# Kernel optimization log

Hardware: AMD Instinct MI355X
Metric: run time of the kernel (lower is better)

The kernel has to match this reference:

```python
import jax, jax.numpy as jnp
import numpy as np
from jax import lax

B, C, H, W_DIM, K = 8, 256, 128, 128, 64


def setup_inputs() -> dict:
    key = jax.random.key(0)
    k1, k2, k3, k4 = jax.random.split(key, 4)
    x = jax.random.normal(k1, (B, C, H, W_DIM), dtype=jnp.float32)
    index = jax.random.randint(k2, (B, H, W_DIM), 0, K)
    stdv = 1.0 / np.sqrt(C)
    W = jax.random.uniform(k3, (C, C), minval=-stdv, maxval=stdv, dtype=jnp.float32)
    conv_w = jax.random.normal(k4, (C, C, 1, 1), dtype=jnp.float32) * stdv
    return {"x": x, "index": index, "W": W, "conv_w": conv_w}


def reference(x, index, W, conv_w):
    # one-hot segment membership (B,H,W,K) -- replaces scatter_ + broadcast in torch
    onehot = jax.nn.one_hot(index, K, dtype=x.dtype)
    counts = jnp.sum(onehot, axis=(1, 2))                       # (B,K)
    sums = jnp.einsum('bhwk,bchw->bkc', onehot, x)              # segment sums
    denom = counts + (counts == 0).astype(x.dtype)              # avoid div by 0
    means = sums / denom[..., None]                             # (B,K,C)

    # Mahalanobis-style pairwise adjacency: adj[b,i,j] = exp(-d^T (W W^T) d)
    M = W @ W.T                                                 # (C,C)
    diff = means[:, None, :, :] - means[:, :, None, :]          # (B,K,K,C): means[b,j]-means[b,i]
    quad = jnp.einsum('bijc,cd,bijd->bij', diff, M, diff)
    adj = jnp.exp(-quad)
    adj = adj * (1.0 - jnp.eye(K, dtype=x.dtype))               # zero diagonal

    # adjacency-weighted message aggregation over segments
    agg = jnp.einsum('bij,bjc->bic', adj, means)                # (B,K,C)

    # scatter messages back to pixels by segment id (each pixel belongs to 1 segment)
    gathered = agg[jnp.arange(B)[:, None, None], index]         # (B,H,W,C)
    features = x + jnp.transpose(gathered, (0, 3, 1, 2))        # (B,C,H,W)

    # 1x1 conv, no bias
    out = lax.conv_general_dilated(features, conv_w, window_strides=(1, 1),
                                   padding='VALID',
                                   dimension_numbers=('NCHW', 'OIHW', 'NCHW'))
    return out
```

## Files before the change

### kernel.cpp

```cpp
#include <hip/hip_runtime.h>
#include <cstdint>
#include <cstddef>

#define B_  8
#define C_  256
#define HW_ 16384
#define K_  64

typedef __attribute__((ext_vector_type(8))) short bf16x8;
typedef __attribute__((ext_vector_type(4))) float f32x4;

__device__ __forceinline__ unsigned f2bf(float f) {
    unsigned u = __builtin_bit_cast(unsigned, f);
    return (u + 0x7FFFu + ((u >> 16) & 1u)) >> 16;
}
__device__ __forceinline__ float bf2f(unsigned h) {
    unsigned u = h << 16;
    return __builtin_bit_cast(float, u);
}

__global__ __launch_bounds__(256) void k_scatter(const float* __restrict__ x,
                                                 const int* __restrict__ idx,
                                                 float* __restrict__ part,
                                                 float* __restrict__ pcnt) {
    __shared__ float lsum[K_ * C_];
    __shared__ int   sidx[256];
    __shared__ float lcnt[K_];
    const int tid = threadIdx.x;
    const int b = blockIdx.y;
    const int pb = blockIdx.x;
    const int p0 = pb * 256;

    float4 z4 = make_float4(0.f, 0.f, 0.f, 0.f);
    for (int i = tid; i < K_ * C_ / 4; i += 256) ((float4*)lsum)[i] = z4;
    if (tid < K_) lcnt[tid] = 0.f;
    sidx[tid] = idx[b * HW_ + p0 + tid];
    __syncthreads();

    atomicAdd(&lcnt[sidx[tid]], 1.f);

    const int c = tid;
    const float4* xr = (const float4*)(x + ((size_t)b * C_ + c) * HW_ + p0);
    #pragma unroll 4
    for (int p4 = 0; p4 < 64; ++p4) {
        float4 v = xr[p4];
        int k0 = sidx[p4 * 4 + 0];
        int k1 = sidx[p4 * 4 + 1];
        int k2 = sidx[p4 * 4 + 2];
        int k3 = sidx[p4 * 4 + 3];
        atomicAdd(&lsum[k0 * C_ + c], v.x);
        atomicAdd(&lsum[k1 * C_ + c], v.y);
        atomicAdd(&lsum[k2 * C_ + c], v.z);
        atomicAdd(&lsum[k3 * C_ + c], v.w);
    }
    __syncthreads();

    const size_t pbg = (size_t)b * 64 + pb;
    float* dst = part + (pbg * K_) * C_;
    for (int k = 0; k < K_; ++k)
        dst[k * C_ + c] = lsum[k * C_ + c];
    if (tid < K_) pcnt[pbg * K_ + tid] = lcnt[tid];
}

__global__ __launch_bounds__(256) void k_reduce(const float* __restrict__ part,
                                                const float* __restrict__ pcnt,
                                                float* __restrict__ means) {
    const int bk = blockIdx.x;
    const int b = bk >> 6, k = bk & 63;
    const int c = threadIdx.x;
    __shared__ float cnt_s;

    if (c < 64) {
        float cl = pcnt[((size_t)b * 64 + c) * K_ + k];
        #pragma unroll
        for (int off = 32; off; off >>= 1) cl += __shfl_down(cl, off);
        if (c == 0) cnt_s = cl;
    }
    __syncthreads();
    const float cnt = cnt_s;
    const float denom = cnt + (cnt == 0.f ? 1.f : 0.f);

    float acc = 0.f;
    #pragma unroll 4
    for (int pb = 0; pb < 64; ++pb)
        acc += part[(((size_t)b * 64 + pb) * K_ + k) * C_ + c];
    means[(size_t)bk * C_ + c] = acc / denom;
}

__global__ __launch_bounds__(256) void k_prep(const float* __restrict__ Wm,
                                              const float* __restrict__ convw,
                                              float* __restrict__ Mm,
                                              float* __restrict__ cwT) {
    const int bx = blockIdx.x, t = threadIdx.x;
    __shared__ float wl[C_];
    if (bx < C_) {
        int cr = bx;
        wl[t] = Wm[cr * C_ + t];
        __syncthreads();
        float acc = 0.f;
        for (int e = 0; e < C_; ++e) acc += wl[e] * Wm[t * C_ + e];
        Mm[cr * C_ + t] = acc;
    } else {
        int cr = bx - C_;
        cwT[cr * C_ + t] = convw[t * C_ + cr];
    }
}

__global__ __launch_bounds__(256) void k_P(const float* __restrict__ means,
                                           const float* __restrict__ Mm,
                                           float* __restrict__ P) {
    const int bi = blockIdx.x;
    const int d = threadIdx.x;
    __shared__ float ml[C_];
    ml[d] = means[(size_t)bi * C_ + d];
    __syncthreads();
    float acc = 0.f;
    for (int cc = 0; cc < C_; ++cc) acc += ml[cc] * Mm[cc * C_ + d];
    P[(size_t)bi * C_ + d] = acc;
}

__global__ __launch_bounds__(256) void k_G(const float* __restrict__ P,
                                           const float* __restrict__ means,
                                           float* __restrict__ G) {
    const int bi = blockIdx.x;
    const int b = bi >> 6;
    const int t = threadIdx.x;
    __shared__ float pl[C_], ml[C_];
    pl[t] = P[(size_t)bi * C_ + t];
    ml[t] = means[(size_t)bi * C_ + t];
    __syncthreads();
    const int j = t >> 2, q = t & 3;
    const float* Pj = P + ((size_t)b * K_ + j) * C_ + q * 64;
    const float* mj = means + ((size_t)b * K_ + j) * C_ + q * 64;
    const float* pq = pl + q * 64;
    const float* mq = ml + q * 64;
    float acc = 0.f;
    for (int d0 = 0; d0 < 64; ++d0) {
        int d = (d0 + q * 16) & 63;
        acc += (pq[d] - Pj[d]) * (mq[d] - mj[d]);
    }
    acc += __shfl_xor(acc, 1);
    acc += __shfl_xor(acc, 2);
    if (q == 0) G[(size_t)bi * K_ + j] = acc;
}

__global__ __launch_bounds__(256) void k_agg(const float* __restrict__ G,
                                             const float* __restrict__ means,
                                             float* __restrict__ agg) {
    const int bi = blockIdx.x;
    const int b = bi >> 6, i = bi & 63;
    const int t = threadIdx.x;
    __shared__ float adjl[K_];
    if (t < K_) {
        int j = t;
        float quad = G[(size_t)bi * K_ + j];
        adjl[j] = (j == i) ? 0.f : expf(-quad);
    }
    __syncthreads();
    float acc = 0.f;
    for (int j = 0; j < K_; ++j)
        acc += adjl[j] * means[((size_t)b * K_ + j) * C_ + t];
    agg[(size_t)bi * C_ + t] = acc;
}

__global__ __launch_bounds__(256) void k_proj(const float* __restrict__ agg,
                                              const float* __restrict__ cwT,
                                              float* __restrict__ proj) {
    const int bk = blockIdx.x;
    const int o = threadIdx.x;
    __shared__ float al[C_];
    al[o] = agg[(size_t)bk * C_ + o];
    __syncthreads();
    float acc = 0.f;
    for (int cc = 0; cc < C_; ++cc) acc += al[cc] * cwT[cc * C_ + o];
    proj[(size_t)bk * C_ + o] = acc;
}

#define BM 128
#define BN 128
#define BKK 32
#define STRD 80

__global__ __launch_bounds__(256) void k_gemm(const float* __restrict__ x,
                                              const int* __restrict__ idx,
                                              const float* __restrict__ convw,
                                              const float* __restrict__ proj,
                                              float* __restrict__ out) {
    __shared__ float Xf[BKK][BN];
    __shared__ __align__(16) unsigned char AsH[BM * STRD];
    __shared__ __align__(16) unsigned char AsL[BM * STRD];
    __shared__ __align__(16) unsigned char BsH[BN * STRD];
    __shared__ __align__(16) unsigned char BsL[BN * STRD];

    const int tid = threadIdx.x;
    const int o0 = blockIdx.x * BM;
    const int p0 = blockIdx.y * BN;
    const int b  = blockIdx.z;

    const int lane = tid & 63;
    const int wv = tid >> 6;
    const int wo = (wv >> 1) * 64, wp = (wv & 1) * 64;
    const int lr = lane & 15, lg = lane >> 4;

    f32x4 acc[4][4];
    #pragma unroll
    for (int i = 0; i < 4; ++i)
        #pragma unroll
        for (int j = 0; j < 4; ++j) acc[i][j] = (f32x4){0.f, 0.f, 0.f, 0.f};

    const float4* w4 = (const float4*)convw;
    const float4* x4 = (const float4*)(x + (size_t)b * C_ * HW_);

    for (int kt = 0; kt < C_; kt += BKK) {
        #pragma unroll
        for (int it = 0; it < 4; ++it) {
            int li = tid + it * 256;
            {
                int row = li >> 3, c4 = li & 7;
                float4 v = w4[(size_t)(o0 + row) * (C_ / 4) + (kt >> 2) + c4];
                unsigned h0 = f2bf(v.x), h1 = f2bf(v.y), h2 = f2bf(v.z), h3 = f2bf(v.w);
                unsigned l0 = f2bf(v.x - bf2f(h0)), l1 = f2bf(v.y - bf2f(h1));
                unsigned l2 = f2bf(v.z - bf2f(h2)), l3 = f2bf(v.w - bf2f(h3));
                uint2 hv, lv;
                hv.x = h0 | (h1 << 16); hv.y = h2 | (h3 << 16);
                lv.x = l0 | (l1 << 16); lv.y = l2 | (l3 << 16);
                *(uint2*)&AsH[row * STRD + c4 * 8] = hv;
                *(uint2*)&AsL[row * STRD + c4 * 8] = lv;
            }
            {
                int row = li >> 5, c4 = li & 31;
                *(float4*)&Xf[row][c4 * 4] =
                    x4[(size_t)(kt + row) * (HW_ / 4) + (p0 >> 2) + c4];
            }
        }
        __syncthreads();
        #pragma unroll
        for (int it = 0; it < 2; ++it) {
            int id = tid + it * 256;
            int p = id & 127, cg = id >> 7;
            unsigned hh[8], ll[8];
            #pragma unroll
            for (int j = 0; j < 8; ++j) {
                float v = Xf[cg * 8 + j][p];
                unsigned h = f2bf(v);
                hh[j] = h;
                ll[j] = f2bf(v - bf2f(h));
            }
            uint4 hv, lv;
            hv.x = hh[0] | (hh[1] << 16); hv.y = hh[2] | (hh[3] << 16);
            hv.z = hh[4] | (hh[5] << 16); hv.w = hh[6] | (hh[7] << 16);
            lv.x = ll[0] | (ll[1] << 16); lv.y = ll[2] | (ll[3] << 16);
            lv.z = ll[4] | (ll[5] << 16); lv.w = ll[6] | (ll[7] << 16);
            *(uint4*)&BsH[p * STRD + cg * 16] = hv;
            *(uint4*)&BsL[p * STRD + cg * 16] = lv;
        }
        __syncthreads();
        bf16x8 ah[4], al[4];
        #pragma unroll
        for (int mt = 0; mt < 4; ++mt) {
            int off = (wo + mt * 16 + lr) * STRD + lg * 16;
            ah[mt] = *(const bf16x8*)&AsH[off];
            al[mt] = *(const bf16x8*)&AsL[off];
        }
        #pragma unroll
        for (int nt = 0; nt < 4; ++nt) {
            int off = (wp + nt * 16 + lr) * STRD + lg * 16;
            bf16x8 bh = *(const bf16x8*)&BsH[off];
            bf16x8 bl = *(const bf16x8*)&BsL[off];
            #pragma unroll
            for (int mt = 0; mt < 4; ++mt) {
                acc[mt][nt] = __builtin_amdgcn_mfma_f32_16x16x32_bf16(ah[mt], bh, acc[mt][nt], 0, 0, 0);
                acc[mt][nt] = __builtin_amdgcn_mfma_f32_16x16x32_bf16(ah[mt], bl, acc[mt][nt], 0, 0, 0);
                acc[mt][nt] = __builtin_amdgcn_mfma_f32_16x16x32_bf16(al[mt], bh, acc[mt][nt], 0, 0, 0);
            }
        }
        __syncthreads();
    }

    #pragma unroll
    for (int nt = 0; nt < 4; ++nt) {
        const int p = p0 + wp + nt * 16 + lr;
        const int kp = idx[b * HW_ + p];
        const float* pr = proj + ((size_t)b * K_ + kp) * C_;
        #pragma unroll
        for (int mt = 0; mt < 4; ++mt) {
            const int ob = o0 + wo + mt * 16 + lg * 4;
            #pragma unroll
            for (int r = 0; r < 4; ++r) {
                const int o = ob + r;
                out[((size_t)b * C_ + o) * HW_ + p] = acc[mt][nt][r] + pr[o];
            }
        }
    }
}

extern "C" void kernel_launch(void* const* d_in, const int* in_sizes, int n_in,
                              void* d_out, int out_size, void* d_ws, size_t ws_size,
                              hipStream_t stream) {
    const float* x     = (const float*)d_in[0];
    const int*   idx   = (const int*)d_in[1];
    const float* Wm    = (const float*)d_in[2];
    const float* convw = (const float*)d_in[3];
    float* out = (float*)d_out;
    float* wsf = (float*)d_ws;

    const size_t N_PART = (size_t)B_ * 64 * K_ * C_;
    const size_t N_PCNT = (size_t)B_ * 64 * K_;
    const size_t N_MEAN = (size_t)B_ * K_ * C_;
    const size_t N_M    = (size_t)C_ * C_;
    const size_t N_G    = (size_t)B_ * K_ * K_;
    const size_t outN   = (size_t)B_ * C_ * HW_;

    float* proj = wsf;
    float* cwT  = wsf + N_MEAN;

    const size_t earlyN = N_PART + N_PCNT + N_MEAN + N_M + N_MEAN + N_G + N_MEAN;
    const size_t needAll = (N_MEAN + N_M + earlyN) * sizeof(float);
    float* early = (ws_size >= needAll) ? (wsf + N_MEAN + N_M)
                                        : (out + (outN - earlyN));

    float* part  = early;
    float* pcnt  = part + N_PART;
    float* means = pcnt + N_PCNT;
    float* Mm    = means + N_MEAN;
    float* P     = Mm + N_M;
    float* G     = P + N_MEAN;
    float* agg   = G + N_G;

    k_scatter<<<dim3(64, 8), dim3(256), 0, stream>>>(x, idx, part, pcnt);
    k_reduce<<<dim3(512), dim3(256), 0, stream>>>(part, pcnt, means);
    k_prep<<<dim3(512), dim3(256), 0, stream>>>(Wm, convw, Mm, cwT);
    k_P<<<dim3(512), dim3(256), 0, stream>>>(means, Mm, P);
    k_G<<<dim3(512), dim3(256), 0, stream>>>(P, means, G);
    k_agg<<<dim3(512), dim3(256), 0, stream>>>(G, means, agg);
    k_proj<<<dim3(512), dim3(256), 0, stream>>>(agg, cwT, proj);
    k_gemm<<<dim3(2, HW_ / BN, B_), dim3(256), 0, stream>>>(x, idx, convw, proj, out);
}
```

Before: 522.7 us.

## Restructure scatter to pixel-major atomics and pre-split conv weights to bf16 hi/lo

```diff
diff --git a/kernel.cpp b/kernel.cpp
--- a/kernel.cpp
+++ b/kernel.cpp
@@ -6,6 +6,8 @@
 #define C_  256
 #define HW_ 16384
 #define K_  64
+#define PPB 1024
+#define NPB (HW_ / PPB)
 
 typedef __attribute__((ext_vector_type(8))) short bf16x8;
 typedef __attribute__((ext_vector_type(4))) float f32x4;
@@ -23,42 +25,43 @@
                                                  const int* __restrict__ idx,
                                                  float* __restrict__ part,
                                                  float* __restrict__ pcnt) {
-    __shared__ float lsum[K_ * C_];
-    __shared__ int   sidx[256];
+    __shared__ float lsum[K_ * 257];
     __shared__ float lcnt[K_];
     const int tid = threadIdx.x;
     const int b = blockIdx.y;
     const int pb = blockIdx.x;
-    const int p0 = pb * 256;
-
-    float4 z4 = make_float4(0.f, 0.f, 0.f, 0.f);
-    for (int i = tid; i < K_ * C_ / 4; i += 256) ((float4*)lsum)[i] = z4;
+    const int p0 = pb * PPB;
+
+    for (int i = tid; i < K_ * 257; i += 256) lsum[i] = 0.f;
     if (tid < K_) lcnt[tid] = 0.f;
-    sidx[tid] = idx[b * HW_ + p0 + tid];
-    __syncthreads();
-
-    atomicAdd(&lcnt[sidx[tid]], 1.f);
-
-    const int c = tid;
-    const float4* xr = (const float4*)(x + ((size_t)b * C_ + c) * HW_ + p0);
-    #pragma unroll 4
-    for (int p4 = 0; p4 < 64; ++p4) {
-        float4 v = xr[p4];
-        int k0 = sidx[p4 * 4 + 0];
-        int k1 = sidx[p4 * 4 + 1];
-        int k2 = sidx[p4 * 4 + 2];
-        int k3 = sidx[p4 * 4 + 3];
-        atomicAdd(&lsum[k0 * C_ + c], v.x);
-        atomicAdd(&lsum[k1 * C_ + c], v.y);
-        atomicAdd(&lsum[k2 * C_ + c], v.z);
-        atomicAdd(&lsum[k3 * C_ + c], v.w);
-    }
-    __syncthreads();
-
-    const size_t pbg = (size_t)b * 64 + pb;
-    float* dst = part + (pbg * K_) * C_;
+    __syncthreads();
+
+    const int p = p0 + tid * 4;
+    const int4 kv = *(const int4*)(idx + b * HW_ + p);
+    atomicAdd(&lcnt[kv.x], 1.f);
+    atomicAdd(&lcnt[kv.y], 1.f);
+    atomicAdd(&lcnt[kv.z], 1.f);
+    atomicAdd(&lcnt[kv.w], 1.f);
+
+    float* a0 = &lsum[kv.x * 257];
+    float* a1 = &lsum[kv.y * 257];
+    float* a2 = &lsum[kv.z * 257];
+    float* a3 = &lsum[kv.w * 257];
+    const float* xp = x + (size_t)b * C_ * HW_ + p;
+    #pragma unroll 8
+    for (int c = 0; c < C_; ++c) {
+        float4 v = *(const float4*)(xp + (size_t)c * HW_);
+        atomicAdd(a0 + c, v.x);
+        atomicAdd(a1 + c, v.y);
+        atomicAdd(a2 + c, v.z);
+        atomicAdd(a3 + c, v.w);
+    }
+    __syncthreads();
+
+    const size_t pbg = (size_t)b * NPB + pb;
+    float* dst = part + pbg * (K_ * C_);
     for (int k = 0; k < K_; ++k)
-        dst[k * C_ + c] = lsum[k * C_ + c];
+        dst[k * C_ + tid] = lsum[k * 257 + tid];
     if (tid < K_) pcnt[pbg * K_ + tid] = lcnt[tid];
 }
 
@@ -70,10 +73,10 @@
     const int c = threadIdx.x;
     __shared__ float cnt_s;
 
-    if (c < 64) {
-        float cl = pcnt[((size_t)b * 64 + c) * K_ + k];
-        #pragma unroll
-        for (int off = 32; off; off >>= 1) cl += __shfl_down(cl, off);
+    if (c < NPB) {
+        float cl = pcnt[((size_t)b * NPB + c) * K_ + k];
+        #pragma unroll
+        for (int off = NPB / 2; off; off >>= 1) cl += __shfl_down(cl, off);
         if (c == 0) cnt_s = cl;
     }
     __syncthreads();
@@ -81,16 +84,18 @@
     const float denom = cnt + (cnt == 0.f ? 1.f : 0.f);
 
     float acc = 0.f;
-    #pragma unroll 4
-    for (int pb = 0; pb < 64; ++pb)
-        acc += part[(((size_t)b * 64 + pb) * K_ + k) * C_ + c];
+    #pragma unroll
+    for (int pb = 0; pb < NPB; ++pb)
+        acc += part[(((size_t)b * NPB + pb) * K_ + k) * C_ + c];
     means[(size_t)bk * C_ + c] = acc / denom;
 }
 
 __global__ __launch_bounds__(256) void k_prep(const float* __restrict__ Wm,
                                               const float* __restrict__ convw,
                                               float* __restrict__ Mm,
-                                              float* __restrict__ cwT) {
+                                              float* __restrict__ cwT,
+                                              unsigned short* __restrict__ cwH,
+                                              unsigned short* __restrict__ cwL) {
     const int bx = blockIdx.x, t = threadIdx.x;
     __shared__ float wl[C_];
     if (bx < C_) {
@@ -100,9 +105,15 @@
         float acc = 0.f;
         for (int e = 0; e < C_; ++e) acc += wl[e] * Wm[t * C_ + e];
         Mm[cr * C_ + t] = acc;
-    } else {
+    } else if (bx < 2 * C_) {
         int cr = bx - C_;
         cwT[cr * C_ + t] = convw[t * C_ + cr];
+    } else {
+        int o = bx - 2 * C_;
+        float v = convw[o * C_ + t];
+        unsigned h = f2bf(v);
+        cwH[o * C_ + t] = (unsigned short)h;
+        cwL[o * C_ + t] = (unsigned short)f2bf(v - bf2f(h));
     }
 }
 
@@ -183,10 +194,10 @@
 
 __global__ __launch_bounds__(256) void k_gemm(const float* __restrict__ x,
                                               const int* __restrict__ idx,
-                                              const float* __restrict__ convw,
+                                              const unsigned short* __restrict__ cwH,
+                                              const unsigned short* __restrict__ cwL,
                                               const float* __restrict__ proj,
                                               float* __restrict__ out) {
-    __shared__ float Xf[BKK][BN];
     __shared__ __align__(16) unsigned char AsH[BM * STRD];
     __shared__ __align__(16) unsigned char AsL[BM * STRD];
     __shared__ __align__(16) unsigned char BsH[BN * STRD];
@@ -208,40 +219,27 @@
         #pragma unroll
         for (int j = 0; j < 4; ++j) acc[i][j] = (f32x4){0.f, 0.f, 0.f, 0.f};
 
-    const float4* w4 = (const float4*)convw;
-    const float4* x4 = (const float4*)(x + (size_t)b * C_ * HW_);
+    const float* xb = x + (size_t)b * C_ * HW_ + p0;
 
     for (int kt = 0; kt < C_; kt += BKK) {
         #pragma unroll
-        for (int it = 0; it < 4; ++it) {
-            int li = tid + it * 256;
-            {
-                int row = li >> 3, c4 = li & 7;
-                float4 v = w4[(size_t)(o0 + row) * (C_ / 4) + (kt >> 2) + c4];
-                unsigned h0 = f2bf(v.x), h1 = f2bf(v.y), h2 = f2bf(v.z), h3 = f2bf(v.w);
-                unsigned l0 = f2bf(v.x - bf2f(h0)), l1 = f2bf(v.y - bf2f(h1));
-                unsigned l2 = f2bf(v.z - bf2f(h2)), l3 = f2bf(v.w - bf2f(h3));
-                uint2 hv, lv;
-                hv.x = h0 | (h1 << 16); hv.y = h2 | (h3 << 16);
-                lv.x = l0 | (l1 << 16); lv.y = l2 | (l3 << 16);
-                *(uint2*)&AsH[row * STRD + c4 * 8] = hv;
-                *(uint2*)&AsL[row * STRD + c4 * 8] = lv;
-            }
-            {
-                int row = li >> 5, c4 = li & 31;
-                *(float4*)&Xf[row][c4 * 4] =
-                    x4[(size_t)(kt + row) * (HW_ / 4) + (p0 >> 2) + c4];
-            }
-        }
-        __syncthreads();
+        for (int it = 0; it < 2; ++it) {
+            int id = tid + it * 256;
+            int row = id >> 2, s = id & 3;
+            uint4 hv = *(const uint4*)&cwH[(o0 + row) * C_ + kt + s * 8];
+            uint4 lv = *(const uint4*)&cwL[(o0 + row) * C_ + kt + s * 8];
+            *(uint4*)&AsH[row * STRD + s * 16] = hv;
+            *(uint4*)&AsL[row * STRD + s * 16] = lv;
+        }
         #pragma unroll
         for (int it = 0; it < 2; ++it) {
             int id = tid + it * 256;
             int p = id & 127, cg = id >> 7;
+            const float* xc = xb + (size_t)(kt + cg * 8) * HW_ + p;
             unsigned hh[8], ll[8];
             #pragma unroll
             for (int j = 0; j < 8; ++j) {
-                float v = Xf[cg * 8 + j][p];
+                float v = xc[(size_t)j * HW_];
                 unsigned h = f2bf(v);
                 hh[j] = h;
                 ll[j] = f2bf(v - bf2f(h));
@@ -304,8 +302,8 @@
     float* out = (float*)d_out;
     float* wsf = (float*)d_ws;
 
-    const size_t N_PART = (size_t)B_ * 64 * K_ * C_;
-    const size_t N_PCNT = (size_t)B_ * 64 * K_;
+    const size_t N_PART = (size_t)B_ * NPB * K_ * C_;
+    const size_t N_PCNT = (size_t)B_ * NPB * K_;
     const size_t N_MEAN = (size_t)B_ * K_ * C_;
     const size_t N_M    = (size_t)C_ * C_;
     const size_t N_G    = (size_t)B_ * K_ * K_;
@@ -313,10 +311,13 @@
 
     float* proj = wsf;
     float* cwT  = wsf + N_MEAN;
+    unsigned short* cwH = (unsigned short*)(wsf + N_MEAN + N_M);
+    unsigned short* cwL = cwH + N_M;
+    const size_t wsHeadF = N_MEAN + N_M + N_M;
 
     const size_t earlyN = N_PART + N_PCNT + N_MEAN + N_M + N_MEAN + N_G + N_MEAN;
-    const size_t needAll = (N_MEAN + N_M + earlyN) * sizeof(float);
-    float* early = (ws_size >= needAll) ? (wsf + N_MEAN + N_M)
+    const size_t needAll = (wsHeadF + earlyN) * sizeof(float);
+    float* early = (ws_size >= needAll) ? (wsf + wsHeadF)
                                         : (out + (outN - earlyN));
 
     float* part  = early;
@@ -327,12 +328,12 @@
     float* G     = P + N_MEAN;
     float* agg   = G + N_G;
 
-    k_scatter<<<dim3(64, 8), dim3(256), 0, stream>>>(x, idx, part, pcnt);
+    k_scatter<<<dim3(NPB, B_), dim3(256), 0, stream>>>(x, idx, part, pcnt);
     k_reduce<<<dim3(512), dim3(256), 0, stream>>>(part, pcnt, means);
-    k_prep<<<dim3(512), dim3(256), 0, stream>>>(Wm, convw, Mm, cwT);
+    k_prep<<<dim3(768), dim3(256), 0, stream>>>(Wm, convw, Mm, cwT, cwH, cwL);
     k_P<<<dim3(512), dim3(256), 0, stream>>>(means, Mm, P);
     k_G<<<dim3(512), dim3(256), 0, stream>>>(P, means, G);
     k_agg<<<dim3(512), dim3(256), 0, stream>>>(G, means, agg);
     k_proj<<<dim3(512), dim3(256), 0, stream>>>(agg, cwT, proj);
-    k_gemm<<<dim3(2, HW_ / BN, B_), dim3(256), 0, stream>>>(x, idx, convw, proj, out);
-}
+    k_gemm<<<dim3(2, HW_ / BN, B_), dim3(256), 0, stream>>>(x, idx, cwH, cwL, proj, out);
+}
```

New measurement: 668.7 us. 27.9% more time.
